# Kernel tuning notes

Measured on AMD Instinct MI355X. Metric: run time of the kernel, lower is better.

## Reference

```python
import jax, jax.numpy as jnp
import numpy as np

B, S, H = 32, 1, 2048
E, I, K = 8, 5632, 2
SWIGLU_SCALE = 1.702


def setup_inputs() -> dict:
    key = jax.random.key(0)
    ks = jax.random.split(key, 5)
    scale_h = 1.0 / np.sqrt(H)
    scale_i = 1.0 / np.sqrt(I)
    return {
        "hidden_states": jax.random.normal(ks[0], (B, S, H), dtype=jnp.float32),
        "router_weight": jax.random.normal(ks[1], (E, H), dtype=jnp.float32) * scale_h,
        "w_gate": jax.random.normal(ks[2], (E, H, I), dtype=jnp.float32) * scale_h,
        "w_up": jax.random.normal(ks[3], (E, H, I), dtype=jnp.float32) * scale_h,
        "w_down": jax.random.normal(ks[4], (E, I, H), dtype=jnp.float32) * scale_i,
        "top_k": K,
    }


def reference(hidden_states, router_weight, w_gate, w_up, w_down, top_k):
    b, s, h = hidden_states.shape
    x = hidden_states.reshape(-1, h)                      # [T, H]
    T = x.shape[0]

    # Router: logits -> softmax affinities -> top-k dispatch weights
    router_logits = x @ router_weight.T                   # [T, E]
    affinities = jax.nn.softmax(router_logits.astype(jnp.float32), axis=-1)
    top_vals, top_idx = jax.lax.top_k(affinities, top_k)  # [T, k]
    # Sparse combine weights: zero except at selected experts
    combine = jnp.zeros_like(affinities).at[jnp.arange(T)[:, None], top_idx].set(top_vals)  # [T, E]

    # Grouped GLU-MLP: dense over all experts (E small), masked combine
    gate = jnp.einsum('th,ehi->tei', x, w_gate)           # [T, E, I]
    up = jnp.einsum('th,ehi->tei', x, w_up)               # [T, E, I]
    inter = gate * jax.nn.sigmoid(SWIGLU_SCALE * gate) * up
    expert_out = jnp.einsum('tei,eih->teh', inter, w_down)  # [T, E, H]

    out = jnp.einsum('te,teh->th', combine.astype(expert_out.dtype), expert_out)
    return out.reshape(b, s, h)
```

## Files before the change

### kernel.cpp

```cpp
#include <hip/hip_runtime.h>
#include <math.h>

#define H_DIM 2048
#define I_DIM 5632
#define E_NUM 8
#define T_NUM 32
#define P_NUM 64
#define GROUP 16
#define HS 8
#define HCH (H_DIM / HS)
#define IS 16
#define ICH (I_DIM / IS)
#define SWIGLU_SCALE 1.702f

__global__ __launch_bounds__(256) void router_kernel(
    const float* __restrict__ x, const float* __restrict__ rw,
    float* __restrict__ combine) {
  const int t = blockIdx.x;
  __shared__ float xs[H_DIM];
  __shared__ float red[4];
  __shared__ float logits[E_NUM];
  for (int h = threadIdx.x; h < H_DIM; h += 256) xs[h] = x[t * H_DIM + h];
  __syncthreads();
  const int lane = threadIdx.x & 63;
  const int wave = threadIdx.x >> 6;
  for (int e = 0; e < E_NUM; ++e) {
    float p = 0.f;
    for (int h = threadIdx.x; h < H_DIM; h += 256) p += xs[h] * rw[e * H_DIM + h];
    for (int off = 32; off; off >>= 1) p += __shfl_down(p, off);
    if (lane == 0) red[wave] = p;
    __syncthreads();
    if (threadIdx.x == 0) logits[e] = red[0] + red[1] + red[2] + red[3];
    __syncthreads();
  }
  if (threadIdx.x == 0) {
    float m = logits[0];
    for (int e = 1; e < E_NUM; ++e) m = fmaxf(m, logits[e]);
    float a[E_NUM]; float s = 0.f;
    for (int e = 0; e < E_NUM; ++e) { a[e] = __expf(logits[e] - m); s += a[e]; }
    const float inv = 1.f / s;
    for (int e = 0; e < E_NUM; ++e) a[e] *= inv;
    int i1 = -1, i2 = -1; float v1 = -1.f, v2 = -1.f;
    for (int e = 0; e < E_NUM; ++e) {
      if (a[e] > v1)      { v2 = v1; i2 = i1; v1 = a[e]; i1 = e; }
      else if (a[e] > v2) { v2 = a[e]; i2 = e; }
    }
    for (int e = 0; e < E_NUM; ++e)
      combine[t * E_NUM + e] = (e == i1) ? v1 : ((e == i2) ? v2 : 0.f);
  }
}

__global__ void compact_kernel(const float* __restrict__ combine,
                               int* __restrict__ cnt, int* __restrict__ start,
                               int* __restrict__ ptok, float* __restrict__ pscale) {
  __shared__ unsigned char flag[T_NUM][E_NUM];
  __shared__ int scnt[E_NUM], sstart[E_NUM];
  const int tid = threadIdx.x;
  {
    const int t = tid >> 3, e = tid & 7;
    flag[t][e] = combine[t * E_NUM + e] > 0.f;
  }
  __syncthreads();
  if (tid < E_NUM) {
    int c = 0;
    for (int t = 0; t < T_NUM; ++t) c += flag[t][tid];
    scnt[tid] = c;
  }
  __syncthreads();
  if (tid == 0) {
    int s = 0;
    for (int e = 0; e < E_NUM; ++e) { sstart[e] = s; s += scnt[e]; }
  }
  __syncthreads();
  if (tid < E_NUM) {
    cnt[tid] = scnt[tid];
    start[tid] = sstart[tid];
    int p = sstart[tid];
    for (int t = 0; t < T_NUM; ++t)
      if (flag[t][tid]) { ptok[p] = t; pscale[p] = combine[t * E_NUM + tid]; ++p; }
  }
  if (tid >= P_NUM && tid < P_NUM + 32) { ptok[tid] = 0; pscale[tid] = 0.f; }
}

template<int EPI>
__global__ __launch_bounds__(256) void gateup_kernel(
    const float* __restrict__ x, const float* __restrict__ wg,
    const float* __restrict__ wu, const int* __restrict__ cnt,
    const int* __restrict__ start, const int* __restrict__ ptok,
    float* __restrict__ pg, float* __restrict__ pu) {
  const int e  = blockIdx.x;
  const int ic = blockIdx.y;
  const int hs = blockIdx.z & (HS - 1);
  const int tg = blockIdx.z >> 3;
  const int c  = cnt[e];
  const int n0 = tg * GROUP;
  if (n0 >= c) return;
  const int nt = min(GROUP, c - n0);
  const int p0 = start[e] + n0;
  const int tid = threadIdx.x;
  const int h0 = hs * HCH;

  __shared__ float xs[GROUP][HCH];
#pragma unroll
  for (int j = 0; j < GROUP; ++j)
    xs[j][tid] = (j < nt) ? x[ptok[p0 + j] * H_DIM + h0 + tid] : 0.f;
  __syncthreads();

  const int i2 = ic * 512 + tid * 2;
  const float* wgp = wg + ((size_t)e * H_DIM + h0) * I_DIM + i2;
  const float* wup = wu + ((size_t)e * H_DIM + h0) * I_DIM + i2;

  float ag[GROUP][2], au[GROUP][2];
#pragma unroll
  for (int j = 0; j < GROUP; ++j) { ag[j][0] = ag[j][1] = au[j][0] = au[j][1] = 0.f; }

#pragma unroll 4
  for (int hh = 0; hh < HCH; ++hh) {
    const float2 g = *(const float2*)(wgp + (size_t)hh * I_DIM);
    const float2 u = *(const float2*)(wup + (size_t)hh * I_DIM);
#pragma unroll
    for (int j = 0; j < GROUP; ++j) {
      const float xv = xs[j][hh];
      ag[j][0] = fmaf(g.x, xv, ag[j][0]);
      ag[j][1] = fmaf(g.y, xv, ag[j][1]);
      au[j][0] = fmaf(u.x, xv, au[j][0]);
      au[j][1] = fmaf(u.y, xv, au[j][1]);
    }
  }

  if (EPI == 0) {
    float* pgp = pg + (size_t)hs * P_NUM * I_DIM;
    float* pup = pu + (size_t)hs * P_NUM * I_DIM;
#pragma unroll
    for (int j = 0; j < GROUP; ++j) if (j < nt) {
      *(float2*)(pgp + (size_t)(p0 + j) * I_DIM + i2) = make_float2(ag[j][0], ag[j][1]);
      *(float2*)(pup + (size_t)(p0 + j) * I_DIM + i2) = make_float2(au[j][0], au[j][1]);
    }
  } else {
#pragma unroll
    for (int j = 0; j < GROUP; ++j) if (j < nt) {
      const size_t o = (size_t)(p0 + j) * I_DIM + i2;
      atomicAdd(&pg[o],     ag[j][0]);
      atomicAdd(&pg[o + 1], ag[j][1]);
      atomicAdd(&pu[o],     au[j][0]);
      atomicAdd(&pu[o + 1], au[j][1]);
    }
  }
}

template<int EPI>
__global__ __launch_bounds__(256) void swiglu_kernel(
    const float* __restrict__ pg, const float* __restrict__ pu,
    const float* __restrict__ pscale, float* __restrict__ inter) {
  const int p = blockIdx.x;
  const int i = blockIdx.y * 256 + threadIdx.x;
  const size_t off = (size_t)p * I_DIM + i;
  float g, u;
  if (EPI == 0) {
    g = 0.f; u = 0.f;
#pragma unroll
    for (int hs = 0; hs < HS; ++hs) {
      g += pg[(size_t)hs * P_NUM * I_DIM + off];
      u += pu[(size_t)hs * P_NUM * I_DIM + off];
    }
  } else {
    g = pg[off]; u = pu[off];
  }
  const float s = pscale[p];
  const float sig = 1.f / (1.f + __expf(-SWIGLU_SCALE * g));
  inter[off] = g * sig * u * s;
}

__global__ __launch_bounds__(256) void down_kernel(
    const float* __restrict__ wd, const float* __restrict__ inter,
    const int* __restrict__ cnt, const int* __restrict__ start,
    const int* __restrict__ ptok, float* __restrict__ out) {
  const int e  = blockIdx.x;
  const int hc = blockIdx.y;
  const int is = blockIdx.z & (IS - 1);
  const int tg = blockIdx.z >> 4;
  const int c  = cnt[e];
  const int n0 = tg * GROUP;
  if (n0 >= c) return;
  const int nt = min(GROUP, c - n0);
  const int p0 = start[e] + n0;
  const int tid = threadIdx.x;
  const int i0 = is * ICH;

  __shared__ float ils[GROUP][ICH];
  for (int idx = tid; idx < GROUP * ICH; idx += 256) {
    const int j = idx / ICH, ii = idx - j * ICH;
    ils[j][ii] = (j < nt) ? inter[(size_t)(p0 + j) * I_DIM + i0 + ii] : 0.f;
  }
  __syncthreads();

  const int h2 = hc * 512 + tid * 2;
  const float* wdp = wd + ((size_t)e * I_DIM + i0) * H_DIM + h2;

  float acc[GROUP][2];
#pragma unroll
  for (int j = 0; j < GROUP; ++j) { acc[j][0] = acc[j][1] = 0.f; }

#pragma unroll 4
  for (int ii = 0; ii < ICH; ++ii) {
    const float2 w = *(const float2*)(wdp + (size_t)ii * H_DIM);
#pragma unroll
    for (int j = 0; j < GROUP; ++j) {
      const float iv = ils[j][ii];
      acc[j][0] = fmaf(w.x, iv, acc[j][0]);
      acc[j][1] = fmaf(w.y, iv, acc[j][1]);
    }
  }

#pragma unroll
  for (int j = 0; j < GROUP; ++j) if (j < nt) {
    const int t = ptok[p0 + j];
    atomicAdd(&out[t * H_DIM + h2],     acc[j][0]);
    atomicAdd(&out[t * H_DIM + h2 + 1], acc[j][1]);
  }
}

extern "C" void kernel_launch(void* const* d_in, const int* in_sizes, int n_in,
                              void* d_out, int out_size, void* d_ws, size_t ws_size,
                              hipStream_t stream) {
  const float* x  = (const float*)d_in[0];
  const float* rw = (const float*)d_in[1];
  const float* wg = (const float*)d_in[2];
  const float* wu = (const float*)d_in[3];
  const float* wd = (const float*)d_in[4];
  float* out = (float*)d_out;

  float* ws      = (float*)d_ws;
  float* combine = ws;
  int*   cnt     = (int*)(ws + 256);
  int*   start   = (int*)(ws + 264);
  int*   ptok    = (int*)(ws + 272);
  float* pscale  = ws + 368;
  float* inter   = ws + 512;
  float* pg      = inter + (size_t)P_NUM * I_DIM;

  const size_t partial_elems = (size_t)HS * P_NUM * I_DIM;
  const size_t need_partial  = (512 + (size_t)P_NUM * I_DIM + 2 * partial_elems) * sizeof(float);
  const bool   use_partial   = ws_size >= need_partial;
  float* pu = pg + (use_partial ? partial_elems : (size_t)P_NUM * I_DIM);

  hipMemsetAsync(d_out, 0, (size_t)out_size * sizeof(float), stream);
  router_kernel<<<T_NUM, 256, 0, stream>>>(x, rw, combine);
  compact_kernel<<<1, 256, 0, stream>>>(combine, cnt, start, ptok, pscale);

  if (use_partial) {
    gateup_kernel<0><<<dim3(E_NUM, I_DIM / 512, HS * 2), 256, 0, stream>>>(
        x, wg, wu, cnt, start, ptok, pg, pu);
    swiglu_kernel<0><<<dim3(P_NUM, I_DIM / 256), 256, 0, stream>>>(pg, pu, pscale, inter);
  } else {
    hipMemsetAsync(pg, 0, 2 * (size_t)P_NUM * I_DIM * sizeof(float), stream);
    gateup_kernel<1><<<dim3(E_NUM, I_DIM / 512, HS * 2), 256, 0, stream>>>(
        x, wg, wu, cnt, start, ptok, pg, pu);
    swiglu_kernel<1><<<dim3(P_NUM, I_DIM / 256), 256, 0, stream>>>(pg, pu, pscale, inter);
  }

  down_kernel<<<dim3(E_NUM, H_DIM / 512, IS * 2), 256, 0, stream>>>(
      wd, inter, cnt, start, ptok, out);
}
```

Before: 268.6 us.

## Fuse router and compaction, widen to float4, replace down atomics with partial-sum combine

Router and compaction are merged into a single 1024-thread kernel that also builds a token-to-pair map. The gate/up, swiglu and down kernels move to 128-thread blocks where each thread handles four columns with float4 loads and stores. The down projection writes per-slice partial sums that a new combine kernel reduces per token, which removes the output memset and the atomics. This aims to cut launch count, atomic contention and load instructions, at the cost of extra workspace traffic for the partials and higher register pressure from 128 accumulators per thread.

```diff
diff --git a/kernel.cpp b/kernel.cpp
--- a/kernel.cpp
+++ b/kernel.cpp
@@ -5,65 +5,55 @@
 #define I_DIM 5632
 #define E_NUM 8
 #define T_NUM 32
+#define K_TOP 2
 #define P_NUM 64
 #define GROUP 16
 #define HS 8
 #define HCH (H_DIM / HS)
 #define IS 16
 #define ICH (I_DIM / IS)
+#define PNI ((size_t)P_NUM * I_DIM)
 #define SWIGLU_SCALE 1.702f
 
-__global__ __launch_bounds__(256) void router_kernel(
+__global__ __launch_bounds__(1024) void route_kernel(
     const float* __restrict__ x, const float* __restrict__ rw,
-    float* __restrict__ combine) {
-  const int t = blockIdx.x;
-  __shared__ float xs[H_DIM];
-  __shared__ float red[4];
-  __shared__ float logits[E_NUM];
-  for (int h = threadIdx.x; h < H_DIM; h += 256) xs[h] = x[t * H_DIM + h];
-  __syncthreads();
-  const int lane = threadIdx.x & 63;
-  const int wave = threadIdx.x >> 6;
-  for (int e = 0; e < E_NUM; ++e) {
+    int* __restrict__ cnt, int* __restrict__ start,
+    int* __restrict__ ptok, float* __restrict__ pscale,
+    int* __restrict__ tpair) {
+  __shared__ float logits[T_NUM][E_NUM];
+  __shared__ int   sidx[T_NUM][K_TOP];
+  __shared__ float sval[T_NUM][K_TOP];
+  __shared__ int   scnt[E_NUM], sstart[E_NUM];
+  __shared__ int   lptok[P_NUM];
+  const int tid = threadIdx.x;
+  const int wave = tid >> 6, lane = tid & 63;
+  for (int k = 0; k < 16; ++k) {
+    const int pair = wave * 16 + k;
+    const int t = pair >> 3, e = pair & 7;
     float p = 0.f;
-    for (int h = threadIdx.x; h < H_DIM; h += 256) p += xs[h] * rw[e * H_DIM + h];
+    for (int h = lane; h < H_DIM; h += 64) p += x[t * H_DIM + h] * rw[e * H_DIM + h];
     for (int off = 32; off; off >>= 1) p += __shfl_down(p, off);
-    if (lane == 0) red[wave] = p;
-    __syncthreads();
-    if (threadIdx.x == 0) logits[e] = red[0] + red[1] + red[2] + red[3];
-    __syncthreads();
-  }
-  if (threadIdx.x == 0) {
-    float m = logits[0];
-    for (int e = 1; e < E_NUM; ++e) m = fmaxf(m, logits[e]);
+    if (lane == 0) logits[t][e] = p;
+  }
+  __syncthreads();
+  if (tid < T_NUM) {
+    float m = logits[tid][0];
+    for (int e = 1; e < E_NUM; ++e) m = fmaxf(m, logits[tid][e]);
     float a[E_NUM]; float s = 0.f;
-    for (int e = 0; e < E_NUM; ++e) { a[e] = __expf(logits[e] - m); s += a[e]; }
+    for (int e = 0; e < E_NUM; ++e) { a[e] = __expf(logits[tid][e] - m); s += a[e]; }
     const float inv = 1.f / s;
-    for (int e = 0; e < E_NUM; ++e) a[e] *= inv;
     int i1 = -1, i2 = -1; float v1 = -1.f, v2 = -1.f;
     for (int e = 0; e < E_NUM; ++e) {
-      if (a[e] > v1)      { v2 = v1; i2 = i1; v1 = a[e]; i1 = e; }
-      else if (a[e] > v2) { v2 = a[e]; i2 = e; }
-    }
-    for (int e = 0; e < E_NUM; ++e)
-      combine[t * E_NUM + e] = (e == i1) ? v1 : ((e == i2) ? v2 : 0.f);
-  }
-}
-
-__global__ void compact_kernel(const float* __restrict__ combine,
-                               int* __restrict__ cnt, int* __restrict__ start,
-                               int* __restrict__ ptok, float* __restrict__ pscale) {
-  __shared__ unsigned char flag[T_NUM][E_NUM];
-  __shared__ int scnt[E_NUM], sstart[E_NUM];
-  const int tid = threadIdx.x;
-  {
-    const int t = tid >> 3, e = tid & 7;
-    flag[t][e] = combine[t * E_NUM + e] > 0.f;
+      const float v = a[e] * inv;
+      if (v > v1)      { v2 = v1; i2 = i1; v1 = v; i1 = e; }
+      else if (v > v2) { v2 = v; i2 = e; }
+    }
+    sidx[tid][0] = i1; sidx[tid][1] = i2; sval[tid][0] = v1; sval[tid][1] = v2;
   }
   __syncthreads();
   if (tid < E_NUM) {
     int c = 0;
-    for (int t = 0; t < T_NUM; ++t) c += flag[t][tid];
+    for (int t = 0; t < T_NUM; ++t) c += (sidx[t][0] == tid) + (sidx[t][1] == tid);
     scnt[tid] = c;
   }
   __syncthreads();
@@ -73,17 +63,22 @@
   }
   __syncthreads();
   if (tid < E_NUM) {
-    cnt[tid] = scnt[tid];
-    start[tid] = sstart[tid];
+    cnt[tid] = scnt[tid]; start[tid] = sstart[tid];
     int p = sstart[tid];
     for (int t = 0; t < T_NUM; ++t)
-      if (flag[t][tid]) { ptok[p] = t; pscale[p] = combine[t * E_NUM + tid]; ++p; }
-  }
-  if (tid >= P_NUM && tid < P_NUM + 32) { ptok[tid] = 0; pscale[tid] = 0.f; }
+      for (int s = 0; s < K_TOP; ++s)
+        if (sidx[t][s] == tid) { ptok[p] = t; pscale[p] = sval[t][s]; lptok[p] = t; ++p; }
+  }
+  __syncthreads();
+  if (tid < T_NUM) {
+    int c2 = 0;
+    for (int p = 0; p < P_NUM; ++p)
+      if (lptok[p] == tid) { tpair[tid * K_TOP + c2] = p; ++c2; }
+  }
 }
 
 template<int EPI>
-__global__ __launch_bounds__(256) void gateup_kernel(
+__global__ __launch_bounds__(128, 2) void gateup_kernel(
     const float* __restrict__ x, const float* __restrict__ wg,
     const float* __restrict__ wu, const int* __restrict__ cnt,
     const int* __restrict__ start, const int* __restrict__ ptok,
@@ -101,80 +96,99 @@
   const int h0 = hs * HCH;
 
   __shared__ float xs[GROUP][HCH];
+  for (int idx = tid; idx < GROUP * HCH; idx += 128) {
+    const int j = idx >> 8, hh = idx & (HCH - 1);
+    xs[j][hh] = (j < nt) ? x[ptok[p0 + j] * H_DIM + h0 + hh] : 0.f;
+  }
+  __syncthreads();
+
+  const int i4 = ic * 512 + tid * 4;
+  const float* wgp = wg + ((size_t)e * H_DIM + h0) * I_DIM + i4;
+  const float* wup = wu + ((size_t)e * H_DIM + h0) * I_DIM + i4;
+
+  float ag[GROUP][4], au[GROUP][4];
 #pragma unroll
   for (int j = 0; j < GROUP; ++j)
-    xs[j][tid] = (j < nt) ? x[ptok[p0 + j] * H_DIM + h0 + tid] : 0.f;
-  __syncthreads();
-
-  const int i2 = ic * 512 + tid * 2;
-  const float* wgp = wg + ((size_t)e * H_DIM + h0) * I_DIM + i2;
-  const float* wup = wu + ((size_t)e * H_DIM + h0) * I_DIM + i2;
-
-  float ag[GROUP][2], au[GROUP][2];
-#pragma unroll
-  for (int j = 0; j < GROUP; ++j) { ag[j][0] = ag[j][1] = au[j][0] = au[j][1] = 0.f; }
-
-#pragma unroll 4
+#pragma unroll
+    for (int q = 0; q < 4; ++q) { ag[j][q] = 0.f; au[j][q] = 0.f; }
+
+#pragma unroll 2
   for (int hh = 0; hh < HCH; ++hh) {
-    const float2 g = *(const float2*)(wgp + (size_t)hh * I_DIM);
-    const float2 u = *(const float2*)(wup + (size_t)hh * I_DIM);
+    const float4 g = *(const float4*)(wgp + (size_t)hh * I_DIM);
+    const float4 u = *(const float4*)(wup + (size_t)hh * I_DIM);
 #pragma unroll
     for (int j = 0; j < GROUP; ++j) {
       const float xv = xs[j][hh];
       ag[j][0] = fmaf(g.x, xv, ag[j][0]);
       ag[j][1] = fmaf(g.y, xv, ag[j][1]);
+      ag[j][2] = fmaf(g.z, xv, ag[j][2]);
+      ag[j][3] = fmaf(g.w, xv, ag[j][3]);
       au[j][0] = fmaf(u.x, xv, au[j][0]);
       au[j][1] = fmaf(u.y, xv, au[j][1]);
+      au[j][2] = fmaf(u.z, xv, au[j][2]);
+      au[j][3] = fmaf(u.w, xv, au[j][3]);
     }
   }
 
   if (EPI == 0) {
-    float* pgp = pg + (size_t)hs * P_NUM * I_DIM;
-    float* pup = pu + (size_t)hs * P_NUM * I_DIM;
+    float* pgp = pg + (size_t)hs * PNI;
+    float* pup = pu + (size_t)hs * PNI;
 #pragma unroll
     for (int j = 0; j < GROUP; ++j) if (j < nt) {
-      *(float2*)(pgp + (size_t)(p0 + j) * I_DIM + i2) = make_float2(ag[j][0], ag[j][1]);
-      *(float2*)(pup + (size_t)(p0 + j) * I_DIM + i2) = make_float2(au[j][0], au[j][1]);
+      const size_t o = (size_t)(p0 + j) * I_DIM + i4;
+      *(float4*)(pgp + o) = make_float4(ag[j][0], ag[j][1], ag[j][2], ag[j][3]);
+      *(float4*)(pup + o) = make_float4(au[j][0], au[j][1], au[j][2], au[j][3]);
     }
   } else {
 #pragma unroll
     for (int j = 0; j < GROUP; ++j) if (j < nt) {
-      const size_t o = (size_t)(p0 + j) * I_DIM + i2;
-      atomicAdd(&pg[o],     ag[j][0]);
-      atomicAdd(&pg[o + 1], ag[j][1]);
-      atomicAdd(&pu[o],     au[j][0]);
-      atomicAdd(&pu[o + 1], au[j][1]);
+      const size_t o = (size_t)(p0 + j) * I_DIM + i4;
+#pragma unroll
+      for (int q = 0; q < 4; ++q) {
+        atomicAdd(&pg[o + q], ag[j][q]);
+        atomicAdd(&pu[o + q], au[j][q]);
+      }
     }
   }
 }
 
 template<int EPI>
-__global__ __launch_bounds__(256) void swiglu_kernel(
+__global__ __launch_bounds__(128) void swiglu_kernel(
     const float* __restrict__ pg, const float* __restrict__ pu,
     const float* __restrict__ pscale, float* __restrict__ inter) {
   const int p = blockIdx.x;
-  const int i = blockIdx.y * 256 + threadIdx.x;
-  const size_t off = (size_t)p * I_DIM + i;
-  float g, u;
+  const int i4 = blockIdx.y * 512 + threadIdx.x * 4;
+  const size_t off = (size_t)p * I_DIM + i4;
+  float g[4] = {0.f, 0.f, 0.f, 0.f}, u[4] = {0.f, 0.f, 0.f, 0.f};
   if (EPI == 0) {
-    g = 0.f; u = 0.f;
 #pragma unroll
     for (int hs = 0; hs < HS; ++hs) {
-      g += pg[(size_t)hs * P_NUM * I_DIM + off];
-      u += pu[(size_t)hs * P_NUM * I_DIM + off];
+      const float4 gv = *(const float4*)(pg + (size_t)hs * PNI + off);
+      const float4 uv = *(const float4*)(pu + (size_t)hs * PNI + off);
+      g[0] += gv.x; g[1] += gv.y; g[2] += gv.z; g[3] += gv.w;
+      u[0] += uv.x; u[1] += uv.y; u[2] += uv.z; u[3] += uv.w;
     }
   } else {
-    g = pg[off]; u = pu[off];
+    const float4 gv = *(const float4*)(pg + off);
+    const float4 uv = *(const float4*)(pu + off);
+    g[0] = gv.x; g[1] = gv.y; g[2] = gv.z; g[3] = gv.w;
+    u[0] = uv.x; u[1] = uv.y; u[2] = uv.z; u[3] = uv.w;
   }
   const float s = pscale[p];
-  const float sig = 1.f / (1.f + __expf(-SWIGLU_SCALE * g));
-  inter[off] = g * sig * u * s;
-}
-
-__global__ __launch_bounds__(256) void down_kernel(
+  float r[4];
+#pragma unroll
+  for (int q = 0; q < 4; ++q) {
+    const float sig = 1.f / (1.f + __expf(-SWIGLU_SCALE * g[q]));
+    r[q] = g[q] * sig * u[q] * s;
+  }
+  *(float4*)(inter + off) = make_float4(r[0], r[1], r[2], r[3]);
+}
+
+template<int EPI>
+__global__ __launch_bounds__(128, 2) void down_kernel(
     const float* __restrict__ wd, const float* __restrict__ inter,
     const int* __restrict__ cnt, const int* __restrict__ start,
-    const int* __restrict__ ptok, float* __restrict__ out) {
+    const int* __restrict__ ptok, float* __restrict__ pout, float* __restrict__ out) {
   const int e  = blockIdx.x;
   const int hc = blockIdx.y;
   const int is = blockIdx.z & (IS - 1);
@@ -188,36 +202,65 @@
   const int i0 = is * ICH;
 
   __shared__ float ils[GROUP][ICH];
-  for (int idx = tid; idx < GROUP * ICH; idx += 256) {
+  for (int idx = tid; idx < GROUP * ICH; idx += 128) {
     const int j = idx / ICH, ii = idx - j * ICH;
     ils[j][ii] = (j < nt) ? inter[(size_t)(p0 + j) * I_DIM + i0 + ii] : 0.f;
   }
   __syncthreads();
 
-  const int h2 = hc * 512 + tid * 2;
-  const float* wdp = wd + ((size_t)e * I_DIM + i0) * H_DIM + h2;
-
-  float acc[GROUP][2];
-#pragma unroll
-  for (int j = 0; j < GROUP; ++j) { acc[j][0] = acc[j][1] = 0.f; }
-
-#pragma unroll 4
+  const int h4 = hc * 512 + tid * 4;
+  const float* wdp = wd + ((size_t)e * I_DIM + i0) * H_DIM + h4;
+
+  float acc[GROUP][4];
+#pragma unroll
+  for (int j = 0; j < GROUP; ++j)
+#pragma unroll
+    for (int q = 0; q < 4; ++q) acc[j][q] = 0.f;
+
+#pragma unroll 2
   for (int ii = 0; ii < ICH; ++ii) {
-    const float2 w = *(const float2*)(wdp + (size_t)ii * H_DIM);
+    const float4 w = *(const float4*)(wdp + (size_t)ii * H_DIM);
 #pragma unroll
     for (int j = 0; j < GROUP; ++j) {
       const float iv = ils[j][ii];
       acc[j][0] = fmaf(w.x, iv, acc[j][0]);
       acc[j][1] = fmaf(w.y, iv, acc[j][1]);
-    }
-  }
-
-#pragma unroll
-  for (int j = 0; j < GROUP; ++j) if (j < nt) {
-    const int t = ptok[p0 + j];
-    atomicAdd(&out[t * H_DIM + h2],     acc[j][0]);
-    atomicAdd(&out[t * H_DIM + h2 + 1], acc[j][1]);
-  }
+      acc[j][2] = fmaf(w.z, iv, acc[j][2]);
+      acc[j][3] = fmaf(w.w, iv, acc[j][3]);
+    }
+  }
+
+  if (EPI == 0) {
+#pragma unroll
+    for (int j = 0; j < GROUP; ++j) if (j < nt) {
+      float* pp = pout + ((size_t)(p0 + j) * IS + is) * H_DIM + h4;
+      *(float4*)pp = make_float4(acc[j][0], acc[j][1], acc[j][2], acc[j][3]);
+    }
+  } else {
+#pragma unroll
+    for (int j = 0; j < GROUP; ++j) if (j < nt) {
+      const int t = ptok[p0 + j];
+#pragma unroll
+      for (int q = 0; q < 4; ++q) atomicAdd(&out[t * H_DIM + h4 + q], acc[j][q]);
+    }
+  }
+}
+
+__global__ __launch_bounds__(256) void combine_kernel(
+    const float* __restrict__ pout, const int* __restrict__ tpair,
+    float* __restrict__ out) {
+  const int t = blockIdx.x;
+  const int h4 = blockIdx.y * 1024 + threadIdx.x * 4;
+  const int pA = tpair[t * K_TOP];
+  const int pB = tpair[t * K_TOP + 1];
+  float s0 = 0.f, s1 = 0.f, s2 = 0.f, s3 = 0.f;
+#pragma unroll
+  for (int is = 0; is < IS; ++is) {
+    const float4 a = *(const float4*)(pout + ((size_t)pA * IS + is) * H_DIM + h4);
+    const float4 b = *(const float4*)(pout + ((size_t)pB * IS + is) * H_DIM + h4);
+    s0 += a.x + b.x; s1 += a.y + b.y; s2 += a.z + b.z; s3 += a.w + b.w;
+  }
+  *(float4*)(out + (size_t)t * H_DIM + h4) = make_float4(s0, s1, s2, s3);
 }
 
 extern "C" void kernel_launch(void* const* d_in, const int* in_sizes, int n_in,
@@ -230,35 +273,38 @@
   const float* wd = (const float*)d_in[4];
   float* out = (float*)d_out;
 
-  float* ws      = (float*)d_ws;
-  float* combine = ws;
-  int*   cnt     = (int*)(ws + 256);
-  int*   start   = (int*)(ws + 264);
-  int*   ptok    = (int*)(ws + 272);
-  float* pscale  = ws + 368;
-  float* inter   = ws + 512;
-  float* pg      = inter + (size_t)P_NUM * I_DIM;
-
-  const size_t partial_elems = (size_t)HS * P_NUM * I_DIM;
-  const size_t need_partial  = (512 + (size_t)P_NUM * I_DIM + 2 * partial_elems) * sizeof(float);
-  const bool   use_partial   = ws_size >= need_partial;
-  float* pu = pg + (use_partial ? partial_elems : (size_t)P_NUM * I_DIM);
-
-  hipMemsetAsync(d_out, 0, (size_t)out_size * sizeof(float), stream);
-  router_kernel<<<T_NUM, 256, 0, stream>>>(x, rw, combine);
-  compact_kernel<<<1, 256, 0, stream>>>(combine, cnt, start, ptok, pscale);
+  float* ws     = (float*)d_ws;
+  int*   cnt    = (int*)ws;
+  int*   start  = (int*)(ws + 8);
+  int*   ptok   = (int*)(ws + 16);
+  int*   tpair  = (int*)(ws + 80);
+  float* pscale = ws + 144;
+  float* inter  = ws + 256;
+  float* pg     = inter + PNI;
+
+  const size_t need_partial =
+      (256 + PNI + 2 * (size_t)HS * PNI + (size_t)P_NUM * IS * H_DIM) * sizeof(float);
+  const bool use_partial = ws_size >= need_partial;
+
+  route_kernel<<<1, 1024, 0, stream>>>(x, rw, cnt, start, ptok, pscale, tpair);
 
   if (use_partial) {
-    gateup_kernel<0><<<dim3(E_NUM, I_DIM / 512, HS * 2), 256, 0, stream>>>(
+    float* pu   = pg + (size_t)HS * PNI;
+    float* pout = pu + (size_t)HS * PNI;
+    gateup_kernel<0><<<dim3(E_NUM, 11, HS * 2), 128, 0, stream>>>(
         x, wg, wu, cnt, start, ptok, pg, pu);
-    swiglu_kernel<0><<<dim3(P_NUM, I_DIM / 256), 256, 0, stream>>>(pg, pu, pscale, inter);
+    swiglu_kernel<0><<<dim3(P_NUM, 11), 128, 0, stream>>>(pg, pu, pscale, inter);
+    down_kernel<0><<<dim3(E_NUM, 4, IS * 2), 128, 0, stream>>>(
+        wd, inter, cnt, start, ptok, pout, out);
+    combine_kernel<<<dim3(T_NUM, 2), 256, 0, stream>>>(pout, tpair, out);
   } else {
-    hipMemsetAsync(pg, 0, 2 * (size_t)P_NUM * I_DIM * sizeof(float), stream);
-    gateup_kernel<1><<<dim3(E_NUM, I_DIM / 512, HS * 2), 256, 0, stream>>>(
+    float* pu = pg + PNI;
+    hipMemsetAsync(out, 0, (size_t)out_size * sizeof(float), stream);
+    hipMemsetAsync(pg, 0, 2 * PNI * sizeof(float), stream);
+    gateup_kernel<1><<<dim3(E_NUM, 11, HS * 2), 128, 0, stream>>>(
         x, wg, wu, cnt, start, ptok, pg, pu);
-    swiglu_kernel<1><<<dim3(P_NUM, I_DIM / 256), 256, 0, stream>>>(pg, pu, pscale, inter);
-  }
-
-  down_kernel<<<dim3(E_NUM, H_DIM / 512, IS * 2), 256, 0, stream>>>(
-      wd, inter, cnt, start, ptok, out);
-}
+    swiglu_kernel<1><<<dim3(P_NUM, 11), 128, 0, stream>>>(pg, pu, pscale, inter);
+    down_kernel<1><<<dim3(E_NUM, 4, IS * 2), 128, 0, stream>>>(
+        wd, inter, cnt, start, ptok, nullptr, out);
+  }
+}
```

Measured after the change: 438.5 us. 63.3% more time.
